# Kernel tuning notes

Hardware: AMD Instinct MI355X
Metric: run time of the kernel (lower is better)

Reference implementation:

```python
import jax, jax.numpy as jnp
import numpy as np

NUM_HEADS = 12
TOP_P = 0.9


def setup_inputs() -> dict:
    key = jax.random.key(0)
    ks = jax.random.split(key, 5)
    B, N, C = 2, 2048, 768
    return {
        "x": jax.random.normal(ks[0], (B, N, C), jnp.float32),
        "qkv_w": jax.random.normal(ks[1], (3 * C, C), jnp.float32) * (C ** -0.5),
        "proj_w": jax.random.normal(ks[2], (C, C), jnp.float32) * (C ** -0.5),
        "proj_b": jax.random.normal(ks[3], (C,), jnp.float32) * 0.02,
        "temperature": jnp.ones((1,), jnp.float32),
        "top_k": 64,
    }


def reference(x, qkv_w, proj_w, proj_b, temperature, top_k):
    B, N, C = x.shape
    H = NUM_HEADS
    D = C // H
    # qkv projection: [B,N,3C] -> [3,B,H,N,D]
    qkv = (x @ qkv_w.T).reshape(B, N, 3, H, D).transpose(2, 0, 3, 1, 4)
    q, k, v = qkv[0], qkv[1], qkv[2]
    scale = (D ** -0.5) * temperature  # (1,) broadcasts
    attn = jnp.einsum("bhnd,bhmd->bhnm", q, k) * scale  # [B,H,N,N]
    neg_inf = jnp.asarray(-jnp.inf, attn.dtype)
    # top-k filtering: keep only scores >= k-th largest per row
    kth = jax.lax.top_k(attn, top_k)[0][..., -1:]
    attn = jnp.where(attn < kth, neg_inf, attn)
    # top-p (nucleus) filtering on sorted scores
    order = jnp.argsort(-attn, axis=-1)  # descending sort indices
    sorted_attn = jnp.take_along_axis(attn, order, axis=-1)
    cum = jnp.cumsum(jax.nn.softmax(sorted_attn, axis=-1), axis=-1)
    rm = cum > TOP_P
    # shift right by one, always keep the top entry
    rm = jnp.concatenate([jnp.zeros_like(rm[..., :1]), rm[..., :-1]], axis=-1)
    # scatter back to original positions via inverse permutation
    inv = jnp.argsort(order, axis=-1)
    remove = jnp.take_along_axis(rm, inv, axis=-1)
    attn = jnp.where(remove, neg_inf, attn)
    p = jax.nn.softmax(attn, axis=-1)
    out = jnp.einsum("bhnm,bhmd->bhnd", p, v)  # [B,H,N,D]
    out = out.transpose(0, 2, 1, 3).reshape(B, N, C)
    return out @ proj_w.T + proj_b
```

## Files before the change

### kernel.cpp

```cpp
#include <hip/hip_runtime.h>
#include <cstdint>

#define NH 12
#define HD 64
#define NSEQ 2048
#define CDIM 768
#define NB 2

__global__ __launch_bounds__(256, 4) void qkv_qk(const float* __restrict__ x,
                                                 const float* __restrict__ w,
                                                 double* __restrict__ Q64,
                                                 double* __restrict__ K64,
                                                 float* __restrict__ Qs32,
                                                 float* __restrict__ Kt32) {
    __shared__ double As[16][128];
    __shared__ double Bs[16][64];
    const int tid = threadIdx.x;
    const int bm = blockIdx.y * 128;
    const int bn = blockIdx.x * 64;
    const int alm = tid >> 1, alk = (tid & 1) * 8;
    const int blm = tid & 63, blk = (tid >> 6) * 4;
    const int tx = tid & 15, ty = tid >> 4;

    double acc[8][4] = {};
    for (int k0 = 0; k0 < CDIM; k0 += 16) {
        float4 a0 = *reinterpret_cast<const float4*>(&x[(bm + alm) * CDIM + k0 + alk]);
        float4 a1 = *reinterpret_cast<const float4*>(&x[(bm + alm) * CDIM + k0 + alk + 4]);
        float4 b0 = *reinterpret_cast<const float4*>(&w[(bn + blm) * CDIM + k0 + blk]);
        __syncthreads();
        As[alk + 0][alm] = (double)a0.x; As[alk + 1][alm] = (double)a0.y;
        As[alk + 2][alm] = (double)a0.z; As[alk + 3][alm] = (double)a0.w;
        As[alk + 4][alm] = (double)a1.x; As[alk + 5][alm] = (double)a1.y;
        As[alk + 6][alm] = (double)a1.z; As[alk + 7][alm] = (double)a1.w;
        Bs[blk + 0][blm] = (double)b0.x; Bs[blk + 1][blm] = (double)b0.y;
        Bs[blk + 2][blm] = (double)b0.z; Bs[blk + 3][blm] = (double)b0.w;
        __syncthreads();
#pragma unroll
        for (int k = 0; k < 16; ++k) {
            double ad[8], bd[4];
#pragma unroll
            for (int i = 0; i < 8; ++i) ad[i] = As[k][ty * 8 + i];
#pragma unroll
            for (int j = 0; j < 4; ++j) bd[j] = Bs[k][tx * 4 + j];
#pragma unroll
            for (int i = 0; i < 8; ++i)
#pragma unroll
                for (int j = 0; j < 4; ++j) acc[i][j] = fma(ad[i], bd[j], acc[i][j]);
        }
        __syncthreads();
    }
    const bool isQ = bn < CDIM;
    const int hh = (isQ ? bn : bn - CDIM) >> 6;
    const int b  = bm >> 11;
    const int bh = b * NH + hh;
#pragma unroll
    for (int i = 0; i < 8; ++i) {
        const int n = (bm + ty * 8 + i) & (NSEQ - 1);
        const size_t base = ((size_t)bh * NSEQ + n) * HD + tx * 4;
        if (isQ) {
            double2 d01; d01.x = acc[i][0]; d01.y = acc[i][1];
            double2 d23; d23.x = acc[i][2]; d23.y = acc[i][3];
            *reinterpret_cast<double2*>(&Q64[base]) = d01;
            *reinterpret_cast<double2*>(&Q64[base + 2]) = d23;
            *reinterpret_cast<float4*>(&Qs32[base]) =
                make_float4((float)acc[i][0], (float)acc[i][1], (float)acc[i][2], (float)acc[i][3]);
        } else {
            double2 d01; d01.x = acc[i][0]; d01.y = acc[i][1];
            double2 d23; d23.x = acc[i][2]; d23.y = acc[i][3];
            *reinterpret_cast<double2*>(&K64[base]) = d01;
            *reinterpret_cast<double2*>(&K64[base + 2]) = d23;
#pragma unroll
            for (int j = 0; j < 4; ++j)
                Kt32[((size_t)bh * HD + tx * 4 + j) * NSEQ + n] = (float)acc[i][j];
        }
    }
}

__global__ __launch_bounds__(256) void qkv_v(const float* __restrict__ x,
                                             const float* __restrict__ wv,
                                             float* __restrict__ V) {
    __shared__ float As[16][64];
    __shared__ float Bs[16][64];
    const int tid = threadIdx.x;
    const int bm = blockIdx.y * 64;
    const int bn = blockIdx.x * 64;
    const int lm = tid >> 2;
    const int lk = (tid & 3) << 2;
    const int tx = tid & 15, ty = tid >> 4;

    float acc[4][4] = {};
    for (int k0 = 0; k0 < CDIM; k0 += 16) {
        float4 av = *reinterpret_cast<const float4*>(&x[(bm + lm) * CDIM + k0 + lk]);
        float4 bv = *reinterpret_cast<const float4*>(&wv[(bn + lm) * CDIM + k0 + lk]);
        __syncthreads();
        As[lk + 0][lm] = av.x; As[lk + 1][lm] = av.y; As[lk + 2][lm] = av.z; As[lk + 3][lm] = av.w;
        Bs[lk + 0][lm] = bv.x; Bs[lk + 1][lm] = bv.y; Bs[lk + 2][lm] = bv.z; Bs[lk + 3][lm] = bv.w;
        __syncthreads();
#pragma unroll
        for (int k = 0; k < 16; ++k) {
            float4 a4 = *reinterpret_cast<const float4*>(&As[k][ty * 4]);
            float4 b4 = *reinterpret_cast<const float4*>(&Bs[k][tx * 4]);
            float aa[4] = {a4.x, a4.y, a4.z, a4.w};
            float bb[4] = {b4.x, b4.y, b4.z, b4.w};
#pragma unroll
            for (int i = 0; i < 4; ++i)
#pragma unroll
                for (int j = 0; j < 4; ++j) acc[i][j] = fmaf(aa[i], bb[j], acc[i][j]);
        }
    }
    const int hh = bn >> 6;
    const int b  = bm >> 11;
#pragma unroll
    for (int i = 0; i < 4; ++i) {
        const int n = (bm + ty * 4 + i) & (NSEQ - 1);
        *reinterpret_cast<float4*>(&V[(((size_t)b * NH + hh) * NSEQ + n) * HD + tx * 4]) =
            make_float4(acc[i][0], acc[i][1], acc[i][2], acc[i][3]);
    }
}

__device__ inline unsigned long long d2key(double f) {
    unsigned long long u = (unsigned long long)__double_as_longlong(f);
    return u ^ (unsigned long long)(((long long)u >> 63) | (long long)0x8000000000000000ull);
}
__device__ inline double key2d(unsigned long long k) {
    unsigned long long mask = ((long long)k < 0) ? 0x8000000000000000ull : 0xFFFFFFFFFFFFFFFFull;
    return __longlong_as_double((long long)(k ^ mask));
}
__device__ inline unsigned kp(float a, float b) {
    unsigned ua = __float_as_uint(a);
    ua ^= (unsigned)(((int)ua >> 31) | 0x80000000);
    unsigned ub = __float_as_uint(b);
    ub ^= (unsigned)(((int)ub >> 31) | 0x80000000);
    return (ua >> 16) | (ub & 0xFFFF0000u);
}

__global__ __launch_bounds__(512, 6) void attn_kernel(const double* __restrict__ Q64,
                                                      const double* __restrict__ K64,
                                                      const float* __restrict__ Qs32,
                                                      const float* __restrict__ Kt32,
                                                      const float* __restrict__ V,
                                                      const float* __restrict__ temp,
                                                      const int* __restrict__ topk_p,
                                                      float* __restrict__ AO) {
    __shared__ unsigned short sk[8][NSEQ];
    __shared__ int cand[8][128];

    const int tid  = threadIdx.x;
    const int bh   = blockIdx.x >> 8;
    const int g0   = (blockIdx.x & 255) << 3;
    const int lane = tid & 63;
    const int wv   = tid >> 6;

    const double scale = 0.125 * (double)temp[0];
    const float sc32 = (float)scale;
    int TK = *topk_p;
    if (TK > 64) TK = 64;
    if (TK < 1)  TK = 1;

    const float* __restrict__ kb = Kt32 + (size_t)bh * HD * NSEQ;
    const float* __restrict__ qp = Qs32 + ((size_t)bh * NSEQ + g0) * HD;
    const int m0 = tid * 4;
    float acc[8][4] = {};
#pragma unroll 4
    for (int d = 0; d < HD; ++d) {
        float4 k4 = *reinterpret_cast<const float4*>(&kb[(size_t)d * NSEQ + m0]);
        float kv[4] = {k4.x, k4.y, k4.z, k4.w};
#pragma unroll
        for (int r8 = 0; r8 < 8; ++r8) {
            float qv = qp[r8 * HD + d];
#pragma unroll
            for (int c = 0; c < 4; ++c) acc[r8][c] = fmaf(qv, kv[c], acc[r8][c]);
        }
    }
#pragma unroll
    for (int r8 = 0; r8 < 8; ++r8) {
        uint2 pkv;
        pkv.x = kp(acc[r8][0] * sc32, acc[r8][1] * sc32);
        pkv.y = kp(acc[r8][2] * sc32, acc[r8][3] * sc32);
        *reinterpret_cast<uint2*>(&sk[r8][m0]) = pkv;
    }
    __syncthreads();

    const int r = wv;
    const int row = g0 + r;

    int k32[32];
#pragma unroll
    for (int i = 0; i < 32; ++i) k32[i] = sk[r][i * 64 + lane];

    int mx = k32[0];
#pragma unroll
    for (int i = 1; i < 32; ++i) mx = max(mx, k32[i]);
#pragma unroll
    for (int off = 32; off > 0; off >>= 1) mx = max(mx, __shfl_xor(mx, off));

    int lo0 = mx > 1024 ? mx - 1024 : 0;
    int c0 = 0;
#pragma unroll
    for (int i = 0; i < 32; ++i) c0 += (int)__popcll(__ballot(k32[i] >= lo0));
    int lo, hi, clo;
    if (c0 >= TK) { lo = lo0; clo = c0; hi = mx; }
    else          { lo = 0;   clo = NSEQ; hi = lo0 - 1; }
    while (lo < hi && clo > 96) {
        int mid = lo + ((hi - lo + 1) >> 1);
        int c = 0;
#pragma unroll
        for (int i = 0; i < 32; ++i) c += (int)__popcll(__ballot(k32[i] >= mid));
        if (c >= TK) { lo = mid; clo = c; } else hi = mid - 1;
    }
    int thr = lo >= 2 ? lo - 2 : 0;

    const unsigned long long lmask = (1ull << lane) - 1ull;
    int base = 0;
#pragma unroll
    for (int i = 0; i < 32; ++i) {
        bool pred = k32[i] >= thr;
        unsigned long long bal = __ballot(pred);
        if (pred) {
            int slot = base + (int)__popcll(bal & lmask);
            if (slot < 128) cand[r][slot] = i * 64 + lane;
        }
        base += (int)__popcll(bal);
    }
    int ncand = min(base, 128);
    asm volatile("s_waitcnt lgkmcnt(0)" ::: "memory");

    const int gidx = lane >> 3;
    const int sl   = lane & 7;
    const double* __restrict__ qrow = Q64 + ((size_t)bh * NSEQ + row) * HD;
    double qd[8];
#pragma unroll
    for (int j = 0; j < 8; ++j) qd[j] = qrow[sl * 8 + j];

    unsigned long long* pkr = reinterpret_cast<unsigned long long*>(&sk[r][0]);
    const double* __restrict__ kbase = K64 + (size_t)bh * NSEQ * HD;
#pragma unroll 2
    for (int jj = 0; jj < 16; ++jj) {
        const int j = (jj + gidx) & 15;
        const int s = gidx * 16 + j;
        const int ms = cand[r][min(s, ncand - 1)];
        const double* __restrict__ kp8 = kbase + (size_t)ms * HD + sl * 8;
        double a = 0.0;
#pragma unroll
        for (int d = 0; d < 8; ++d) a = fma(qd[d], kp8[d], a);
        a += __shfl_xor(a, 1);
        a += __shfl_xor(a, 2);
        a += __shfl_xor(a, 4);
        a *= scale;
        unsigned long long pkv = (s < ncand)
            ? ((d2key(a) & ~2047ull) | (unsigned long long)(2047 - ms)) : 0ull;
        if (sl == (jj & 7)) pkr[s] = pkv;
    }
    asm volatile("s_waitcnt lgkmcnt(0)" ::: "memory");
    unsigned long long pk1 = pkr[lane];
    unsigned long long pk2 = pkr[64 + lane];

    unsigned long long t0 = ~pk1, t1 = ~pk2;
#pragma unroll
    for (int k = 2; k <= 64; k <<= 1) {
#pragma unroll
        for (int j = k >> 1; j > 0; j >>= 1) {
            {
                unsigned long long ot = __shfl_xor(t0, j);
                bool dir = (lane & k) != 0;
                bool lower = (lane & j) == 0;
                bool takeMin = (lower != dir);
                bool less = t0 < ot;
                t0 = (takeMin == less) ? t0 : ot;
            }
            {
                unsigned long long ot = __shfl_xor(t1, j);
                bool dir = (k == 64) ? true : ((lane & k) != 0);
                bool lower = (lane & j) == 0;
                bool takeMin = (lower != dir);
                bool less = t1 < ot;
                t1 = (takeMin == less) ? t1 : ot;
            }
        }
    }
    {
        unsigned long long na = (t1 < t0) ? t1 : t0;
        unsigned long long nb = (t1 < t0) ? t0 : t1;
        t0 = na; t1 = nb;
    }
#pragma unroll
    for (int j = 32; j > 0; j >>= 1) {
        {
            unsigned long long ot = __shfl_xor(t0, j);
            bool lower = (lane & j) == 0;
            bool less = t0 < ot;
            t0 = (lower == less) ? t0 : ot;
        }
        {
            unsigned long long ot = __shfl_xor(t1, j);
            bool lower = (lane & j) == 0;
            bool less = t1 < ot;
            t1 = (lower == less) ? t1 : ot;
        }
    }
    unsigned long long kk = ~t0;
    int mi = 2047 - (int)(kk & 2047ull);
    bool valid = lane < TK;
    double a = valid ? key2d(kk & ~2047ull) : 0.0;
    double amax = __shfl(a, 0);
    double s = valid ? exp(a - amax) : 0.0;

    double ps = s;
#pragma unroll
    for (int off = 1; off < 64; off <<= 1) {
        double tt = __shfl_up(ps, off);
        if (lane >= off) ps += tt;
    }
    double S = __shfl(ps, 63);
    double cumprev = (ps - s) / S;
    bool keep = valid && ((lane == 0) || (cumprev <= 0.9));
    double sk2 = keep ? s : 0.0;
    double S2 = sk2;
#pragma unroll
    for (int off = 32; off > 0; off >>= 1) S2 += __shfl_xor(S2, off);
    float p = (float)(keep ? (s / S2) : 0.0);

    unsigned long long bal = __ballot(keep);
    int nk = __popcll(bal);

    const float* __restrict__ vb = V + (size_t)bh * NSEQ * HD;
    float o = 0.f;
    for (int i = 0; i < nk; ++i) {
        float pi = __shfl(p, i);
        int midx = __shfl(mi, i);
        o = fmaf(pi, vb[(size_t)midx * HD + lane], o);
    }
    const int b = bh / NH, hh = bh % NH;
    AO[((size_t)b * NSEQ + row) * CDIM + hh * HD + lane] = o;
}

__global__ __launch_bounds__(256) void proj_gemm(const float* __restrict__ A,
                                                 const float* __restrict__ w,
                                                 const float* __restrict__ bias,
                                                 float* __restrict__ out) {
    __shared__ float As[16][128];
    __shared__ float Bs[16][64];
    const int tid = threadIdx.x;
    const int bm = blockIdx.y * 128;
    const int bn = blockIdx.x * 64;
    const int alm = tid >> 1, alk = (tid & 1) * 8;
    const int blm = tid & 63, blk = (tid >> 6) * 4;
    const int tx = tid & 15, ty = tid >> 4;

    float acc[8][4] = {};
    for (int k0 = 0; k0 < CDIM; k0 += 16) {
        float4 a0 = *reinterpret_cast<const float4*>(&A[(bm + alm) * CDIM + k0 + alk]);
        float4 a1 = *reinterpret_cast<const float4*>(&A[(bm + alm) * CDIM + k0 + alk + 4]);
        float4 b0 = *reinterpret_cast<const float4*>(&w[(bn + blm) * CDIM + k0 + blk]);
        __syncthreads();
        As[alk + 0][alm] = a0.x; As[alk + 1][alm] = a0.y;
        As[alk + 2][alm] = a0.z; As[alk + 3][alm] = a0.w;
        As[alk + 4][alm] = a1.x; As[alk + 5][alm] = a1.y;
        As[alk + 6][alm] = a1.z; As[alk + 7][alm] = a1.w;
        Bs[blk + 0][blm] = b0.x; Bs[blk + 1][blm] = b0.y;
        Bs[blk + 2][blm] = b0.z; Bs[blk + 3][blm] = b0.w;
        __syncthreads();
#pragma unroll
        for (int k = 0; k < 16; ++k) {
            float4 af0 = *reinterpret_cast<const float4*>(&As[k][ty * 8]);
            float4 af1 = *reinterpret_cast<const float4*>(&As[k][ty * 8 + 4]);
            float4 bf  = *reinterpret_cast<const float4*>(&Bs[k][tx * 4]);
            float aa[8] = {af0.x, af0.y, af0.z, af0.w, af1.x, af1.y, af1.z, af1.w};
            float bb[4] = {bf.x, bf.y, bf.z, bf.w};
#pragma unroll
            for (int i = 0; i < 8; ++i)
#pragma unroll
                for (int j = 0; j < 4; ++j) acc[i][j] = fmaf(aa[i], bb[j], acc[i][j]);
        }
        __syncthreads();
    }
    float4 bv = *reinterpret_cast<const float4*>(&bias[bn + tx * 4]);
#pragma unroll
    for (int i = 0; i < 8; ++i) {
        int rr = bm + ty * 8 + i;
        float4 v4 = make_float4(acc[i][0] + bv.x, acc[i][1] + bv.y,
                                acc[i][2] + bv.z, acc[i][3] + bv.w);
        *reinterpret_cast<float4*>(&out[(size_t)rr * CDIM + bn + tx * 4]) = v4;
    }
}

extern "C" void kernel_launch(void* const* d_in, const int* in_sizes, int n_in,
                              void* d_out, int out_size, void* d_ws, size_t ws_size,
                              hipStream_t stream) {
    const float* x      = (const float*)d_in[0];
    const float* qkv_w  = (const float*)d_in[1];
    const float* proj_w = (const float*)d_in[2];
    const float* proj_b = (const float*)d_in[3];
    const float* temp   = (const float*)d_in[4];
    const int*   topk   = (const int*)d_in[5];
    float* out = (float*)d_out;

    const size_t HSZ = (size_t)NB * NH * NSEQ * HD;
    double* Q64  = (double*)d_ws;
    double* K64  = Q64 + HSZ;
    float*  Qs32 = (float*)(K64 + HSZ);
    float*  Kt32 = Qs32 + HSZ;
    float*  V    = Kt32 + HSZ;
    float*  AO   = V + HSZ;

    qkv_qk<<<dim3(24, 32), 256, 0, stream>>>(x, qkv_w, Q64, K64, Qs32, Kt32);
    qkv_v<<<dim3(12, 64), 256, 0, stream>>>(x, qkv_w + (size_t)2 * CDIM * CDIM, V);
    attn_kernel<<<dim3(NB * NH * (NSEQ / 8)), 512, 0, stream>>>(Q64, K64, Qs32, Kt32, V, temp, topk, AO);
    proj_gemm<<<dim3(12, 32), 256, 0, stream>>>(AO, proj_w, proj_b, out);
}
```

Before: 790.9 us.

## Enlarge QK projection tile to 128x128 and trim candidate rescoring loop

The fp64 Q/K projection GEMM now uses a 128x128 output tile with an 8x8 per-thread accumulator and interleaved column ownership, which halves the grid and raises arithmetic intensity per shared-memory load. The output stores become scalar per-element writes instead of vector double2/float4 stores. In the attention kernel, the candidate rescoring loop now runs only as many iterations as needed for the actual candidate count, with the packed-key buffer zeroed up front, instead of always running 16 iterations. Costs are higher register pressure (occupancy hint lowered to 2) and less coalesced stores.

```diff
diff --git a/kernel.cpp b/kernel.cpp
--- a/kernel.cpp
+++ b/kernel.cpp
@@ -7,71 +7,70 @@
 #define CDIM 768
 #define NB 2
 
-__global__ __launch_bounds__(256, 4) void qkv_qk(const float* __restrict__ x,
+__global__ __launch_bounds__(256, 2) void qkv_qk(const float* __restrict__ x,
                                                  const float* __restrict__ w,
                                                  double* __restrict__ Q64,
                                                  double* __restrict__ K64,
                                                  float* __restrict__ Qs32,
                                                  float* __restrict__ Kt32) {
     __shared__ double As[16][128];
-    __shared__ double Bs[16][64];
+    __shared__ double Bs[16][128];
     const int tid = threadIdx.x;
     const int bm = blockIdx.y * 128;
-    const int bn = blockIdx.x * 64;
-    const int alm = tid >> 1, alk = (tid & 1) * 8;
-    const int blm = tid & 63, blk = (tid >> 6) * 4;
+    const int bn = blockIdx.x * 128;
+    const int lm = tid & 127;
+    const int lk = (tid >> 7) * 8;
     const int tx = tid & 15, ty = tid >> 4;
 
-    double acc[8][4] = {};
+    double acc[8][8] = {};
     for (int k0 = 0; k0 < CDIM; k0 += 16) {
-        float4 a0 = *reinterpret_cast<const float4*>(&x[(bm + alm) * CDIM + k0 + alk]);
-        float4 a1 = *reinterpret_cast<const float4*>(&x[(bm + alm) * CDIM + k0 + alk + 4]);
-        float4 b0 = *reinterpret_cast<const float4*>(&w[(bn + blm) * CDIM + k0 + blk]);
-        __syncthreads();
-        As[alk + 0][alm] = (double)a0.x; As[alk + 1][alm] = (double)a0.y;
-        As[alk + 2][alm] = (double)a0.z; As[alk + 3][alm] = (double)a0.w;
-        As[alk + 4][alm] = (double)a1.x; As[alk + 5][alm] = (double)a1.y;
-        As[alk + 6][alm] = (double)a1.z; As[alk + 7][alm] = (double)a1.w;
-        Bs[blk + 0][blm] = (double)b0.x; Bs[blk + 1][blm] = (double)b0.y;
-        Bs[blk + 2][blm] = (double)b0.z; Bs[blk + 3][blm] = (double)b0.w;
+        float4 a0 = *reinterpret_cast<const float4*>(&x[(bm + lm) * CDIM + k0 + lk]);
+        float4 a1 = *reinterpret_cast<const float4*>(&x[(bm + lm) * CDIM + k0 + lk + 4]);
+        float4 b0 = *reinterpret_cast<const float4*>(&w[(bn + lm) * CDIM + k0 + lk]);
+        float4 b1 = *reinterpret_cast<const float4*>(&w[(bn + lm) * CDIM + k0 + lk + 4]);
+        __syncthreads();
+        As[lk + 0][lm] = (double)a0.x; As[lk + 1][lm] = (double)a0.y;
+        As[lk + 2][lm] = (double)a0.z; As[lk + 3][lm] = (double)a0.w;
+        As[lk + 4][lm] = (double)a1.x; As[lk + 5][lm] = (double)a1.y;
+        As[lk + 6][lm] = (double)a1.z; As[lk + 7][lm] = (double)a1.w;
+        Bs[lk + 0][lm] = (double)b0.x; Bs[lk + 1][lm] = (double)b0.y;
+        Bs[lk + 2][lm] = (double)b0.z; Bs[lk + 3][lm] = (double)b0.w;
+        Bs[lk + 4][lm] = (double)b1.x; Bs[lk + 5][lm] = (double)b1.y;
+        Bs[lk + 6][lm] = (double)b1.z; Bs[lk + 7][lm] = (double)b1.w;
         __syncthreads();
 #pragma unroll
         for (int k = 0; k < 16; ++k) {
-            double ad[8], bd[4];
+            double ad[8], bd[8];
 #pragma unroll
             for (int i = 0; i < 8; ++i) ad[i] = As[k][ty * 8 + i];
 #pragma unroll
-            for (int j = 0; j < 4; ++j) bd[j] = Bs[k][tx * 4 + j];
+            for (int j = 0; j < 8; ++j) bd[j] = Bs[k][j * 16 + tx];
 #pragma unroll
             for (int i = 0; i < 8; ++i)
 #pragma unroll
-                for (int j = 0; j < 4; ++j) acc[i][j] = fma(ad[i], bd[j], acc[i][j]);
-        }
-        __syncthreads();
-    }
-    const bool isQ = bn < CDIM;
-    const int hh = (isQ ? bn : bn - CDIM) >> 6;
-    const int b  = bm >> 11;
-    const int bh = b * NH + hh;
+                for (int j = 0; j < 8; ++j) acc[i][j] = fma(ad[i], bd[j], acc[i][j]);
+        }
+        __syncthreads();
+    }
+    const int b = bm >> 11;
 #pragma unroll
     for (int i = 0; i < 8; ++i) {
         const int n = (bm + ty * 8 + i) & (NSEQ - 1);
-        const size_t base = ((size_t)bh * NSEQ + n) * HD + tx * 4;
-        if (isQ) {
-            double2 d01; d01.x = acc[i][0]; d01.y = acc[i][1];
-            double2 d23; d23.x = acc[i][2]; d23.y = acc[i][3];
-            *reinterpret_cast<double2*>(&Q64[base]) = d01;
-            *reinterpret_cast<double2*>(&Q64[base + 2]) = d23;
-            *reinterpret_cast<float4*>(&Qs32[base]) =
-                make_float4((float)acc[i][0], (float)acc[i][1], (float)acc[i][2], (float)acc[i][3]);
-        } else {
-            double2 d01; d01.x = acc[i][0]; d01.y = acc[i][1];
-            double2 d23; d23.x = acc[i][2]; d23.y = acc[i][3];
-            *reinterpret_cast<double2*>(&K64[base]) = d01;
-            *reinterpret_cast<double2*>(&K64[base + 2]) = d23;
-#pragma unroll
-            for (int j = 0; j < 4; ++j)
-                Kt32[((size_t)bh * HD + tx * 4 + j) * NSEQ + n] = (float)acc[i][j];
+#pragma unroll
+        for (int j = 0; j < 8; ++j) {
+            const int col = bn + j * 16 + tx;
+            if (col < CDIM) {
+                const int hh = col >> 6, d = col & 63;
+                const size_t base = (((size_t)(b * NH + hh)) * NSEQ + n) * HD + d;
+                Q64[base]  = acc[i][j];
+                Qs32[base] = (float)acc[i][j];
+            } else {
+                const int ck = col - CDIM;
+                const int hh = ck >> 6, d = ck & 63;
+                const int bh = b * NH + hh;
+                K64[(((size_t)bh) * NSEQ + n) * HD + d] = acc[i][j];
+                Kt32[((size_t)bh * HD + d) * NSEQ + n]  = (float)acc[i][j];
+            }
         }
     }
 }
@@ -233,11 +232,12 @@
     for (int j = 0; j < 8; ++j) qd[j] = qrow[sl * 8 + j];
 
     unsigned long long* pkr = reinterpret_cast<unsigned long long*>(&sk[r][0]);
+    pkr[lane] = 0ull;
+    pkr[64 + lane] = 0ull;
     const double* __restrict__ kbase = K64 + (size_t)bh * NSEQ * HD;
-#pragma unroll 2
-    for (int jj = 0; jj < 16; ++jj) {
-        const int j = (jj + gidx) & 15;
-        const int s = gidx * 16 + j;
+    const int jmax = (ncand + 7) >> 3;
+    for (int j = 0; j < jmax; ++j) {
+        const int s = j * 8 + gidx;
         const int ms = cand[r][min(s, ncand - 1)];
         const double* __restrict__ kp8 = kbase + (size_t)ms * HD + sl * 8;
         double a = 0.0;
@@ -247,9 +247,8 @@
         a += __shfl_xor(a, 2);
         a += __shfl_xor(a, 4);
         a *= scale;
-        unsigned long long pkv = (s < ncand)
-            ? ((d2key(a) & ~2047ull) | (unsigned long long)(2047 - ms)) : 0ull;
-        if (sl == (jj & 7)) pkr[s] = pkv;
+        unsigned long long pkv = (d2key(a) & ~2047ull) | (unsigned long long)(2047 - ms);
+        if (sl == (j & 7) && s < ncand) pkr[s] = pkv;
     }
     asm volatile("s_waitcnt lgkmcnt(0)" ::: "memory");
     unsigned long long pk1 = pkr[lane];
@@ -403,7 +402,7 @@
     float*  V    = Kt32 + HSZ;
     float*  AO   = V + HSZ;
 
-    qkv_qk<<<dim3(24, 32), 256, 0, stream>>>(x, qkv_w, Q64, K64, Qs32, Kt32);
+    qkv_qk<<<dim3(12, 32), 256, 0, stream>>>(x, qkv_w, Q64, K64, Qs32, Kt32);
     qkv_v<<<dim3(12, 64), 256, 0, stream>>>(x, qkv_w + (size_t)2 * CDIM * CDIM, V);
     attn_kernel<<<dim3(NB * NH * (NSEQ / 8)), 512, 0, stream>>>(Q64, K64, Qs32, Kt32, V, temp, topk, AO);
     proj_gemm<<<dim3(12, 32), 256, 0, stream>>>(AO, proj_w, proj_b, out);
```

After: 840.3 us. 6.3% more time.
